# Optimization experiments

Hardware: AMD Instinct MI355X
Metric: run time of the kernel (lower is better)

## Reference

```python
import jax, jax.numpy as jnp
import numpy as np

LN_EPS = 1e-5

def setup_inputs() -> dict:
    key = jax.random.key(0)
    ks = jax.random.split(key, 8)
    B, L, D, H = 4, 2048, 512, 8
    x = jax.random.normal(ks[0], (B, L, D), dtype=jnp.float32)
    token_ids = jax.random.randint(ks[1], (B, L), 0, 50000, dtype=jnp.int64)
    s = 1.0 / np.sqrt(D)
    Wq = jax.random.normal(ks[2], (D, D), dtype=jnp.float32) * s
    Wk = jax.random.normal(ks[3], (D, D), dtype=jnp.float32) * s
    Wv = jax.random.normal(ks[4], (D, D), dtype=jnp.float32) * s
    Wo = jax.random.normal(ks[5], (D, D), dtype=jnp.float32) * s
    gamma = jnp.ones((D,), dtype=jnp.float32)
    beta = jnp.zeros((D,), dtype=jnp.float32)
    return {"x": x, "token_ids": token_ids, "Wq": Wq, "Wk": Wk,
            "Wv": Wv, "Wo": Wo, "gamma": gamma, "beta": beta}

def reference(x, token_ids, Wq, Wk, Wv, Wo, gamma, beta):
    B, L, D = x.shape
    H = 8
    Dh = D // H
    residual = x
    # Pre-LN
    mu = jnp.mean(x, axis=-1, keepdims=True)
    var = jnp.mean(jnp.square(x - mu), axis=-1, keepdims=True)
    xn = (x - mu) * jax.lax.rsqrt(var + LN_EPS) * gamma + beta
    # projections (torch Linear: y = x @ W.T), split heads -> [B,H,L,Dh]
    def proj(W):
        return jnp.einsum('bld,ed->ble', xn, W).reshape(B, L, H, Dh).transpose(0, 2, 1, 3)
    Q, K, V = proj(Wq), proj(Wk), proj(Wv)
    scale = jnp.sqrt(jnp.float32(Dh))
    scores = jnp.einsum('bhqd,bhkd->bhqk', Q, K) / scale  # [B,H,L,L]
    neg_inf = jnp.float32(-jnp.inf)
    causal = jnp.triu(jnp.ones((L, L), dtype=bool), k=1)           # [L,L]
    pad = (token_ids == 0)[:, None, None, :]                       # [B,1,1,L]
    scores = jnp.where(causal[None, None], neg_inf, scores)
    scores = jnp.where(pad, neg_inf, scores)
    all_masked = jnp.all(jnp.isinf(scores), axis=-1, keepdims=True)
    scores = jnp.where(all_masked, 0.0, scores)
    attn = jax.nn.softmax(scores, axis=-1)  # dropout is identity in eval
    out = jnp.einsum('bhqk,bhkd->bhqd', attn, V)
    out = out.transpose(0, 2, 1, 3).reshape(B, L, D)
    out = jnp.einsum('bld,ed->ble', out, Wo)
    return residual + out
```

## Files before the change

### kernel.cpp

```cpp
#include <hip/hip_runtime.h>
#include <math.h>

typedef unsigned short u16;
typedef unsigned int u32;
typedef unsigned long long u64;
typedef float f32x4 __attribute__((ext_vector_type(4)));
typedef __bf16 bf16x8 __attribute__((ext_vector_type(8)));
typedef __bf16 bf16x4 __attribute__((ext_vector_type(4)));

constexpr int Bc = 4, Lc = 2048, Dc = 512, Hc = 8, DHc = 64;
constexpr int NTOK = Bc * Lc;
constexpr float LN_EPS = 1e-5f;
constexpr int KS = 72;
constexpr int PS = 72;
constexpr float QSCALE = 0.125f * 1.44269504088896340736f;

__device__ inline u16 bf_bits(float f) {
  return __builtin_bit_cast(u16, (__bf16)f);
}

__global__ __launch_bounds__(256) void cvt4_kernel(const float* __restrict__ s0,
                                                   const float* __restrict__ s1,
                                                   const float* __restrict__ s2,
                                                   const float* __restrict__ s3,
                                                   u16* __restrict__ d0,
                                                   u16* __restrict__ d1,
                                                   u16* __restrict__ d2,
                                                   u16* __restrict__ d3) {
  int mat = blockIdx.x >> 8;
  int i = ((blockIdx.x & 255) * 256 + threadIdx.x) * 4;
  const float* s = (mat == 0) ? s0 : (mat == 1) ? s1 : (mat == 2) ? s2 : s3;
  u16* d = (mat == 0) ? d0 : (mat == 1) ? d1 : (mat == 2) ? d2 : d3;
  float4 v = *(const float4*)&s[i];
  bf16x4 o;
  o[0] = (__bf16)v.x; o[1] = (__bf16)v.y; o[2] = (__bf16)v.z; o[3] = (__bf16)v.w;
  *(bf16x4*)&d[i] = o;
}

__global__ __launch_bounds__(256) void pmask_kernel(const int* __restrict__ tok,
                                                    u64* __restrict__ pm) {
  int wid = (blockIdx.x * 256 + threadIdx.x) >> 6;
  int lane = threadIdx.x & 63;
  u64 m = __ballot(tok[(size_t)wid * 64 + lane] == 0);
  if (lane == 0) pm[wid] = m;
}

__global__ __launch_bounds__(256) void ln_kernel(const float* __restrict__ x,
                                                 const float* __restrict__ gamma,
                                                 const float* __restrict__ beta,
                                                 u16* __restrict__ xn) {
  int wave = threadIdx.x >> 6;
  int lane = threadIdx.x & 63;
  int row  = blockIdx.x * 4 + wave;
  const float* xr = x + (size_t)row * Dc;
  float4 v0 = ((const float4*)xr)[lane * 2];
  float4 v1 = ((const float4*)xr)[lane * 2 + 1];
  float sum = v0.x + v0.y + v0.z + v0.w + v1.x + v1.y + v1.z + v1.w;
  float sq  = v0.x*v0.x + v0.y*v0.y + v0.z*v0.z + v0.w*v0.w
            + v1.x*v1.x + v1.y*v1.y + v1.z*v1.z + v1.w*v1.w;
  #pragma unroll
  for (int off = 32; off > 0; off >>= 1) {
    sum += __shfl_xor(sum, off);
    sq  += __shfl_xor(sq, off);
  }
  float mu = sum * (1.0f / Dc);
  float rs = rsqrtf(sq * (1.0f / Dc) - mu * mu + LN_EPS);
  float4 g0 = ((const float4*)gamma)[lane * 2];
  float4 g1 = ((const float4*)gamma)[lane * 2 + 1];
  float4 b0 = ((const float4*)beta)[lane * 2];
  float4 b1 = ((const float4*)beta)[lane * 2 + 1];
  bf16x8 o;
  o[0] = (__bf16)((v0.x - mu) * rs * g0.x + b0.x);
  o[1] = (__bf16)((v0.y - mu) * rs * g0.y + b0.y);
  o[2] = (__bf16)((v0.z - mu) * rs * g0.z + b0.z);
  o[3] = (__bf16)((v0.w - mu) * rs * g0.w + b0.w);
  o[4] = (__bf16)((v1.x - mu) * rs * g1.x + b1.x);
  o[5] = (__bf16)((v1.y - mu) * rs * g1.y + b1.y);
  o[6] = (__bf16)((v1.z - mu) * rs * g1.z + b1.z);
  o[7] = (__bf16)((v1.w - mu) * rs * g1.w + b1.w);
  *(bf16x8*)&xn[(size_t)row * Dc + lane * 8] = o;
}

template <int MODE>
__global__ __launch_bounds__(256) void gemm_bf16(const u16* __restrict__ A,
                                                 const u16* __restrict__ W,
                                                 const float* __restrict__ res,
                                                 float* __restrict__ out_f,
                                                 u16* __restrict__ o_q,
                                                 u16* __restrict__ o_k,
                                                 u16* __restrict__ o_v,
                                                 float* __restrict__ vm) {
  __shared__ u16 As[128 * KS];
  __shared__ u16 Bs[128 * KS];
  int tid = threadIdx.x;
  int lane = tid & 63;
  int w = tid >> 6;
  int wr = w >> 1, wc = w & 1;
  int cc = lane & 15, rb = lane >> 4;
  int n0 = blockIdx.x * 128;
  int e0 = blockIdx.y * 128;
  f32x4 acc[4][4] = {};
  for (int k0 = 0; k0 < Dc; k0 += 64) {
    #pragma unroll
    for (int u = 0; u < 4; u++) {
      int idx = u * 256 + tid;
      int row = idx >> 3;
      int col = (idx & 7) << 3;
      *(uint4*)&As[row * KS + col] = *(const uint4*)&A[(size_t)(n0 + row) * Dc + k0 + col];
      *(uint4*)&Bs[row * KS + col] = *(const uint4*)&W[(size_t)(e0 + row) * Dc + k0 + col];
    }
    __syncthreads();
    #pragma unroll
    for (int kk = 0; kk < 64; kk += 32) {
      bf16x8 aF[4], bF[4];
      #pragma unroll
      for (int m = 0; m < 4; m++)
        aF[m] = *(bf16x8*)&As[(wr * 64 + m * 16 + cc) * KS + kk + rb * 8];
      #pragma unroll
      for (int n = 0; n < 4; n++)
        bF[n] = *(bf16x8*)&Bs[(wc * 64 + n * 16 + cc) * KS + kk + rb * 8];
      #pragma unroll
      for (int m = 0; m < 4; m++)
        #pragma unroll
        for (int n = 0; n < 4; n++)
          acc[m][n] = __builtin_amdgcn_mfma_f32_16x16x32_bf16(aF[m], bF[n], acc[m][n], 0, 0, 0);
    }
    __syncthreads();
  }
  if (MODE == 3) {
    int bb = n0 >> 11;
    #pragma unroll
    for (int n = 0; n < 4; n++) {
      int c = e0 + wc * 64 + n * 16 + cc;
      int mat = c >> 9;
      int cm = c & 511;
      int h = cm >> 6, dh = cm & 63;
      if (mat == 2) {
        float cp = 0.f;
        #pragma unroll
        for (int m = 0; m < 4; m++) {
          int l0 = (n0 + wr * 64 + m * 16 + rb * 4) & (Lc - 1);
          bf16x4 o4;
          o4[0] = (__bf16)acc[m][n][0]; o4[1] = (__bf16)acc[m][n][1];
          o4[2] = (__bf16)acc[m][n][2]; o4[3] = (__bf16)acc[m][n][3];
          *(bf16x4*)&o_v[((size_t)(bb * Hc + h) * DHc + dh) * Lc + l0] = o4;
          cp += (acc[m][n][0] + acc[m][n][1]) + (acc[m][n][2] + acc[m][n][3]);
        }
        cp += __shfl_xor(cp, 16);
        cp += __shfl_xor(cp, 32);
        if (lane < 16) atomicAdd(&vm[(bb * Hc + h) * DHc + dh], cp);
      } else {
        u16* dst = (mat == 0) ? o_q : o_k;
        float sc = (mat == 0) ? QSCALE : 1.0f;
        #pragma unroll
        for (int m = 0; m < 4; m++) {
          #pragma unroll
          for (int j = 0; j < 4; j++) {
            int r = n0 + wr * 64 + m * 16 + rb * 4 + j;
            int ll = r & (Lc - 1);
            dst[(((size_t)(bb * Hc + h)) * Lc + ll) * DHc + dh] = bf_bits(acc[m][n][j] * sc);
          }
        }
      }
    }
  } else {
    #pragma unroll
    for (int m = 0; m < 4; m++) {
      #pragma unroll
      for (int n = 0; n < 4; n++) {
        #pragma unroll
        for (int j = 0; j < 4; j++) {
          int r = n0 + wr * 64 + m * 16 + rb * 4 + j;
          int c = e0 + wc * 64 + n * 16 + cc;
          size_t o = (size_t)r * Dc + c;
          out_f[o] = acc[m][n][j] + res[o];
        }
      }
    }
  }
}

__global__ __launch_bounds__(64) void attn3(const u16* __restrict__ Q,
                                            const u16* __restrict__ K,
                                            const u16* __restrict__ VT,
                                            const float* __restrict__ vm,
                                            const u64* __restrict__ pmask,
                                            u16* __restrict__ out) {
  __shared__ u16 Ps[32 * PS];
  int lane = threadIdx.x;
  int cc = lane & 15, rb = lane >> 4;
  int bh = blockIdx.x;
  int qt = (int)gridDim.y - 1 - (int)blockIdx.y;
  int q0 = qt * 32;
  int b = bh >> 3, h = bh & 7;
  const u16* Qb = Q + (size_t)bh * Lc * DHc;
  const u16* Kb = K + (size_t)bh * Lc * DHc;
  const u16* Vb = VT + (size_t)bh * DHc * Lc;
  const u64* pmb = pmask + (b << 5);

  bf16x8 qF[2][2];
  #pragma unroll
  for (int qb = 0; qb < 2; qb++)
    #pragma unroll
    for (int kc = 0; kc < 2; kc++)
      qF[qb][kc] = *(const bf16x8*)&Qb[(size_t)(q0 + qb * 16 + cc) * DHc + kc * 32 + rb * 8];

  float mrow[2] = {-INFINITY, -INFINITY};
  float lrow[2] = {0.f, 0.f};
  f32x4 acc[2][4] = {};
  int nfull = q0 >> 6;

  bf16x8 kf[4][2];
  #pragma unroll
  for (int c = 0; c < 4; c++) {
    const u16* kp = &Kb[(size_t)(c * 16 + cc) * DHc + rb * 8];
    kf[c][0] = *(const bf16x8*)kp;
    kf[c][1] = *(const bf16x8*)(kp + 32);
  }

  for (int kt = 0; kt <= nfull; kt++) {
    int k0 = kt * 64;
    bool last = (kt == nfull);
    u64 pm = pmb[kt];
    bf16x8 vf[2][4];
    #pragma unroll
    for (int kc = 0; kc < 2; kc++)
      #pragma unroll
      for (int d0 = 0; d0 < 4; d0++)
        vf[kc][d0] = *(const bf16x8*)&Vb[(size_t)(d0 * 16 + cc) * Lc + k0 + kc * 32 + rb * 8];

    f32x4 sq[2][4] = {};
    __builtin_amdgcn_s_setprio(1);
    #pragma unroll
    for (int c = 0; c < 4; c++) {
      #pragma unroll
      for (int qb = 0; qb < 2; qb++) {
        sq[qb][c] = __builtin_amdgcn_mfma_f32_16x16x32_bf16(kf[c][0], qF[qb][0], sq[qb][c], 0, 0, 0);
        sq[qb][c] = __builtin_amdgcn_mfma_f32_16x16x32_bf16(kf[c][1], qF[qb][1], sq[qb][c], 0, 0, 0);
      }
    }
    __builtin_amdgcn_s_setprio(0);
    if (!last) {
      #pragma unroll
      for (int c = 0; c < 4; c++) {
        const u16* kp = &Kb[(size_t)(k0 + 64 + c * 16 + cc) * DHc + rb * 8];
        kf[c][0] = *(const bf16x8*)kp;
        kf[c][1] = *(const bf16x8*)(kp + 32);
      }
    }
    #pragma unroll
    for (int c = 0; c < 4; c++) {
      u32 smr = (((u32)(pm >> (c * 16)) & 0xffffu) >> (rb * 4));
      #pragma unroll
      for (int qb = 0; qb < 2; qb++)
        #pragma unroll
        for (int j = 0; j < 4; j++)
          if ((smr >> j) & 1) sq[qb][c][j] = -INFINITY;
    }
    if (last) {
      #pragma unroll
      for (int qb = 0; qb < 2; qb++) {
        int qrel = q0 + qb * 16 + cc - k0;
        #pragma unroll
        for (int c = 0; c < 4; c++)
          #pragma unroll
          for (int j = 0; j < 4; j++)
            if (c * 16 + rb * 4 + j > qrel) sq[qb][c][j] = -INFINITY;
      }
    }
    #pragma unroll
    for (int qb = 0; qb < 2; qb++) {
      float m0 = fmaxf(fmaxf(sq[qb][0][0], sq[qb][0][1]), fmaxf(sq[qb][0][2], sq[qb][0][3]));
      float m1 = fmaxf(fmaxf(sq[qb][1][0], sq[qb][1][1]), fmaxf(sq[qb][1][2], sq[qb][1][3]));
      float m2 = fmaxf(fmaxf(sq[qb][2][0], sq[qb][2][1]), fmaxf(sq[qb][2][2], sq[qb][2][3]));
      float m3 = fmaxf(fmaxf(sq[qb][3][0], sq[qb][3][1]), fmaxf(sq[qb][3][2], sq[qb][3][3]));
      float mx = fmaxf(fmaxf(m0, m1), fmaxf(m2, m3));
      mx = fmaxf(mx, __shfl_xor(mx, 16));
      mx = fmaxf(mx, __shfl_xor(mx, 32));
      if (!__all(mx <= mrow[qb] + 8.f)) {
        float nm = fmaxf(mrow[qb], mx);
        float nm2 = fmaxf(nm, -1e30f);
        float alpha = exp2f(mrow[qb] - nm2);
        lrow[qb] *= alpha;
        #pragma unroll
        for (int d0 = 0; d0 < 4; d0++)
          #pragma unroll
          for (int j = 0; j < 4; j++)
            acc[qb][d0][j] *= alpha;
        mrow[qb] = nm;
      }
      float nm2 = fmaxf(mrow[qb], -1e30f);
      float rs = 0.f;
      #pragma unroll
      for (int c = 0; c < 4; c++) {
        f32x4 p;
        #pragma unroll
        for (int j = 0; j < 4; j++) p[j] = exp2f(sq[qb][c][j] - nm2);
        rs += (p[0] + p[1]) + (p[2] + p[3]);
        bf16x4 p4;
        p4[0] = (__bf16)p[0]; p4[1] = (__bf16)p[1];
        p4[2] = (__bf16)p[2]; p4[3] = (__bf16)p[3];
        *(bf16x4*)&Ps[(qb * 16 + cc) * PS + c * 16 + rb * 4] = p4;
      }
      rs += __shfl_xor(rs, 16);
      rs += __shfl_xor(rs, 32);
      lrow[qb] += rs;
    }
    asm volatile("s_waitcnt lgkmcnt(0)" ::: "memory");
    __builtin_amdgcn_sched_barrier(0);
    __builtin_amdgcn_s_setprio(1);
    #pragma unroll
    for (int kc = 0; kc < 2; kc++) {
      bf16x8 pF0 = *(bf16x8*)&Ps[(size_t)cc * PS + kc * 32 + rb * 8];
      bf16x8 pF1 = *(bf16x8*)&Ps[(size_t)(16 + cc) * PS + kc * 32 + rb * 8];
      #pragma unroll
      for (int d0 = 0; d0 < 4; d0++) {
        acc[0][d0] = __builtin_amdgcn_mfma_f32_16x16x32_bf16(vf[kc][d0], pF0, acc[0][d0], 0, 0, 0);
        acc[1][d0] = __builtin_amdgcn_mfma_f32_16x16x32_bf16(vf[kc][d0], pF1, acc[1][d0], 0, 0, 0);
      }
    }
    __builtin_amdgcn_s_setprio(0);
  }
  #pragma unroll
  for (int qb = 0; qb < 2; qb++) {
    int q = q0 + qb * 16 + cc;
    bool ok = lrow[qb] > 0.f;
    float inv = ok ? 1.0f / lrow[qb] : 0.f;
    #pragma unroll
    for (int d0 = 0; d0 < 4; d0++) {
      bf16x4 o4;
      #pragma unroll
      for (int j = 0; j < 4; j++) {
        float v = ok ? acc[qb][d0][j] * inv
                     : vm[bh * DHc + d0 * 16 + rb * 4 + j] * (1.0f / Lc);
        o4[j] = (__bf16)v;
      }
      *(bf16x4*)&out[((size_t)(b * Lc + q)) * Dc + h * DHc + d0 * 16 + rb * 4] = o4;
    }
  }
}

extern "C" void kernel_launch(void* const* d_in, const int* in_sizes, int n_in,
                              void* d_out, int out_size, void* d_ws, size_t ws_size,
                              hipStream_t stream) {
  const float* x     = (const float*)d_in[0];
  const int*   tok   = (const int*)d_in[1];
  const float* Wq    = (const float*)d_in[2];
  const float* Wk    = (const float*)d_in[3];
  const float* Wv    = (const float*)d_in[4];
  const float* Wo    = (const float*)d_in[5];
  const float* gamma = (const float*)d_in[6];
  const float* beta  = (const float*)d_in[7];
  float* out = (float*)d_out;

  const size_t SEG = (size_t)NTOK * Dc;
  const size_t WSEG = (size_t)Dc * Dc;
  u16* xn   = (u16*)d_ws;
  u16* Qd   = xn + SEG;
  u16* Kd   = Qd + SEG;
  u16* VT   = Kd + SEG;
  u16* ao   = VT + SEG;
  u16* Wqkv = ao + SEG;
  u16* Wob  = Wqkv + 3 * WSEG;
  float* vm = (float*)(Wob + WSEG);
  u64* pmarr = (u64*)(vm + (size_t)Bc * Hc * DHc);

  (void)hipMemsetAsync(vm, 0, (size_t)Bc * Hc * DHc * sizeof(float), stream);

  cvt4_kernel<<<1024, 256, 0, stream>>>(Wq, Wk, Wv, Wo,
                                        Wqkv, Wqkv + WSEG, Wqkv + 2 * WSEG, Wob);
  ln_kernel<<<NTOK / 4, 256, 0, stream>>>(x, gamma, beta, xn);
  pmask_kernel<<<32, 256, 0, stream>>>(tok, pmarr);

  dim3 gq(NTOK / 128, (3 * Dc) / 128);
  gemm_bf16<3><<<gq, 256, 0, stream>>>(xn, Wqkv, nullptr, nullptr, Qd, Kd, VT, vm);

  dim3 ga(Bc * Hc, Lc / 32);
  attn3<<<ga, 64, 0, stream>>>(Qd, Kd, VT, vm, pmarr, ao);

  dim3 gg(NTOK / 128, Dc / 128);
  gemm_bf16<0><<<gg, 256, 0, stream>>>(ao, Wob, x, out, nullptr, nullptr, nullptr, nullptr);
}
```

Baseline: 123.5 us.

## Share K/V tiles across four waves via double-buffered async LDS staging

The attention kernel goes from one wave per 32-query tile to four waves per 128-query block. The waves share K and V tiles staged into XOR-swizzled LDS with async global_load_lds double buffering, instead of each wave reading K/V from global memory itself. The V projection output is rewritten into a 64x64-blocked transposed layout so each tile is one contiguous 8KB chunk, and the weight-convert and pad-mask kernels are merged into one launch. This cuts redundant global K/V traffic and one launch. In exchange it adds per-tile block barriers, and waves with fewer causal tiles sit idle while their neighbours finish.

```diff
diff --git a/kernel.cpp b/kernel.cpp
--- a/kernel.cpp
+++ b/kernel.cpp
@@ -19,30 +19,32 @@
   return __builtin_bit_cast(u16, (__bf16)f);
 }
 
-__global__ __launch_bounds__(256) void cvt4_kernel(const float* __restrict__ s0,
+__global__ __launch_bounds__(256) void prep_kernel(const float* __restrict__ s0,
                                                    const float* __restrict__ s1,
                                                    const float* __restrict__ s2,
                                                    const float* __restrict__ s3,
                                                    u16* __restrict__ d0,
                                                    u16* __restrict__ d1,
                                                    u16* __restrict__ d2,
-                                                   u16* __restrict__ d3) {
-  int mat = blockIdx.x >> 8;
-  int i = ((blockIdx.x & 255) * 256 + threadIdx.x) * 4;
-  const float* s = (mat == 0) ? s0 : (mat == 1) ? s1 : (mat == 2) ? s2 : s3;
-  u16* d = (mat == 0) ? d0 : (mat == 1) ? d1 : (mat == 2) ? d2 : d3;
-  float4 v = *(const float4*)&s[i];
-  bf16x4 o;
-  o[0] = (__bf16)v.x; o[1] = (__bf16)v.y; o[2] = (__bf16)v.z; o[3] = (__bf16)v.w;
-  *(bf16x4*)&d[i] = o;
-}
-
-__global__ __launch_bounds__(256) void pmask_kernel(const int* __restrict__ tok,
-                                                    u64* __restrict__ pm) {
-  int wid = (blockIdx.x * 256 + threadIdx.x) >> 6;
-  int lane = threadIdx.x & 63;
-  u64 m = __ballot(tok[(size_t)wid * 64 + lane] == 0);
-  if (lane == 0) pm[wid] = m;
+                                                   u16* __restrict__ d3,
+                                                   const int* __restrict__ tok,
+                                                   u64* __restrict__ pm) {
+  int bid = blockIdx.x;
+  if (bid < 1024) {
+    int mat = bid >> 8;
+    int i = ((bid & 255) * 256 + threadIdx.x) * 4;
+    const float* s = (mat == 0) ? s0 : (mat == 1) ? s1 : (mat == 2) ? s2 : s3;
+    u16* d = (mat == 0) ? d0 : (mat == 1) ? d1 : (mat == 2) ? d2 : d3;
+    float4 v = *(const float4*)&s[i];
+    bf16x4 o;
+    o[0] = (__bf16)v.x; o[1] = (__bf16)v.y; o[2] = (__bf16)v.z; o[3] = (__bf16)v.w;
+    *(bf16x4*)&d[i] = o;
+  } else {
+    int wid = ((bid - 1024) * 256 + threadIdx.x) >> 6;
+    int lane = threadIdx.x & 63;
+    u64 m = __ballot(tok[(size_t)wid * 64 + lane] == 0);
+    if (lane == 0) pm[wid] = m;
+  }
 }
 
 __global__ __launch_bounds__(256) void ln_kernel(const float* __restrict__ x,
@@ -129,36 +131,41 @@
   }
   if (MODE == 3) {
     int bb = n0 >> 11;
-    #pragma unroll
-    for (int n = 0; n < 4; n++) {
-      int c = e0 + wc * 64 + n * 16 + cc;
-      int mat = c >> 9;
-      int cm = c & 511;
-      int h = cm >> 6, dh = cm & 63;
-      if (mat == 2) {
+    int mat = e0 >> 9;
+    int e0c = e0 & 511;
+    if (mat == 2) {
+      #pragma unroll
+      for (int n = 0; n < 4; n++) {
+        int c = e0c + wc * 64 + n * 16 + cc;
+        int h = c >> 6, dh = c & 63;
         float cp = 0.f;
         #pragma unroll
         for (int m = 0; m < 4; m++) {
-          int l0 = (n0 + wr * 64 + m * 16 + rb * 4) & (Lc - 1);
+          int l = (n0 + wr * 64 + m * 16 + rb * 4) & (Lc - 1);
           bf16x4 o4;
           o4[0] = (__bf16)acc[m][n][0]; o4[1] = (__bf16)acc[m][n][1];
           o4[2] = (__bf16)acc[m][n][2]; o4[3] = (__bf16)acc[m][n][3];
-          *(bf16x4*)&o_v[((size_t)(bb * Hc + h) * DHc + dh) * Lc + l0] = o4;
+          size_t addr = ((((size_t)(bb * Hc + h)) * (Lc / 64) + (l >> 6)) * DHc + dh) * 64 + (l & 63);
+          *(bf16x4*)&o_v[addr] = o4;
           cp += (acc[m][n][0] + acc[m][n][1]) + (acc[m][n][2] + acc[m][n][3]);
         }
         cp += __shfl_xor(cp, 16);
         cp += __shfl_xor(cp, 32);
         if (lane < 16) atomicAdd(&vm[(bb * Hc + h) * DHc + dh], cp);
-      } else {
-        u16* dst = (mat == 0) ? o_q : o_k;
-        float sc = (mat == 0) ? QSCALE : 1.0f;
-        #pragma unroll
-        for (int m = 0; m < 4; m++) {
+      }
+    } else {
+      float sc = (mat == 0) ? QSCALE : 1.0f;
+      u16* dst = (mat == 0) ? o_q : o_k;
+      #pragma unroll
+      for (int m = 0; m < 4; m++) {
+        #pragma unroll
+        for (int n = 0; n < 4; n++) {
           #pragma unroll
           for (int j = 0; j < 4; j++) {
             int r = n0 + wr * 64 + m * 16 + rb * 4 + j;
+            int c = e0c + wc * 64 + n * 16 + cc;
             int ll = r & (Lc - 1);
-            dst[(((size_t)(bb * Hc + h)) * Lc + ll) * DHc + dh] = bf_bits(acc[m][n][j] * sc);
+            dst[(((size_t)(bb * Hc + (c >> 6))) * Lc + ll) * DHc + (c & 63)] = bf_bits(acc[m][n][j] * sc);
           }
         }
       }
@@ -180,23 +187,29 @@
   }
 }
 
-__global__ __launch_bounds__(64) void attn3(const u16* __restrict__ Q,
-                                            const u16* __restrict__ K,
-                                            const u16* __restrict__ VT,
-                                            const float* __restrict__ vm,
-                                            const u64* __restrict__ pmask,
-                                            u16* __restrict__ out) {
-  __shared__ u16 Ps[32 * PS];
-  int lane = threadIdx.x;
+__global__ __launch_bounds__(256) void attn5(const u16* __restrict__ Q,
+                                             const u16* __restrict__ K,
+                                             const u16* __restrict__ VT,
+                                             const float* __restrict__ vm,
+                                             const u64* __restrict__ pmask,
+                                             u16* __restrict__ out) {
+  __shared__ u16 Ksh[2][4096];
+  __shared__ u16 Vsh[2][4096];
+  __shared__ u16 Ps[4][32 * PS];
+  int tid = threadIdx.x;
+  int w = tid >> 6;
+  int lane = tid & 63;
   int cc = lane & 15, rb = lane >> 4;
   int bh = blockIdx.x;
-  int qt = (int)gridDim.y - 1 - (int)blockIdx.y;
-  int q0 = qt * 32;
+  int qblk = (int)gridDim.y - 1 - (int)blockIdx.y;
+  int q0 = qblk * 128 + w * 32;
   int b = bh >> 3, h = bh & 7;
   const u16* Qb = Q + (size_t)bh * Lc * DHc;
   const u16* Kb = K + (size_t)bh * Lc * DHc;
-  const u16* Vb = VT + (size_t)bh * DHc * Lc;
+  const u16* Vb = VT + (size_t)bh * Lc * DHc;
   const u64* pmb = pmask + (b << 5);
+  int own_last = q0 >> 6;
+  int NT = 2 * qblk + 2;
 
   bf16x8 qF[2][2];
   #pragma unroll
@@ -208,119 +221,137 @@
   float mrow[2] = {-INFINITY, -INFINITY};
   float lrow[2] = {0.f, 0.f};
   f32x4 acc[2][4] = {};
-  int nfull = q0 >> 6;
-
-  bf16x8 kf[4][2];
-  #pragma unroll
-  for (int c = 0; c < 4; c++) {
-    const u16* kp = &Kb[(size_t)(c * 16 + cc) * DHc + rb * 8];
-    kf[c][0] = *(const bf16x8*)kp;
-    kf[c][1] = *(const bf16x8*)(kp + 32);
-  }
-
-  for (int kt = 0; kt <= nfull; kt++) {
-    int k0 = kt * 64;
-    bool last = (kt == nfull);
-    u64 pm = pmb[kt];
-    bf16x8 vf[2][4];
-    #pragma unroll
-    for (int kc = 0; kc < 2; kc++)
-      #pragma unroll
-      for (int d0 = 0; d0 < 4; d0++)
-        vf[kc][d0] = *(const bf16x8*)&Vb[(size_t)(d0 * 16 + cc) * Lc + k0 + kc * 32 + rb * 8];
-
-    f32x4 sq[2][4] = {};
-    __builtin_amdgcn_s_setprio(1);
-    #pragma unroll
-    for (int c = 0; c < 4; c++) {
+
+  auto stage = [&](int kt, int buf) {
+    const char* gK = (const char*)(Kb + (size_t)kt * 64 * DHc);
+    const char* gV = (const char*)(Vb + (size_t)kt * 4096);
+    #pragma unroll
+    for (int i = 0; i < 2; i++) {
+      int s = (i * 4 + w) * 64 + lane;
+      int row = s >> 3;
+      int src = row * 128 + (((s & 7) ^ (row & 7)) << 4);
+      u16* lK = &Ksh[buf][(i * 4 + w) * 512];
+      u16* lV = &Vsh[buf][(i * 4 + w) * 512];
+      __builtin_amdgcn_global_load_lds(
+          (const __attribute__((address_space(1))) void*)(gK + src),
+          (__attribute__((address_space(3))) void*)lK, 16, 0, 0);
+      __builtin_amdgcn_global_load_lds(
+          (const __attribute__((address_space(1))) void*)(gV + src),
+          (__attribute__((address_space(3))) void*)lV, 16, 0, 0);
+    }
+  };
+
+  stage(0, 0);
+  for (int kt = 0; kt < NT; kt++) {
+    int cur = kt & 1;
+    bool more = (kt + 1 < NT);
+    if (more) stage(kt + 1, cur ^ 1);
+    if (more) asm volatile("s_waitcnt vmcnt(4)" ::: "memory");
+    else      asm volatile("s_waitcnt vmcnt(0)" ::: "memory");
+    __builtin_amdgcn_sched_barrier(0);
+    __builtin_amdgcn_s_barrier();
+    __builtin_amdgcn_sched_barrier(0);
+
+    if (kt <= own_last) {
+      const u16* Kl = Ksh[cur];
+      const u16* Vl = Vsh[cur];
+      bool last = (kt == own_last);
+      u64 pm = pmb[kt];
+      int sw = cc & 7;
+      f32x4 sq[2][4] = {};
+      #pragma unroll
+      for (int c = 0; c < 4; c++) {
+        int krow = c * 16 + cc;
+        bf16x8 kf0 = *(const bf16x8*)&Kl[krow * 64 + ((rb ^ sw) << 3)];
+        bf16x8 kf1 = *(const bf16x8*)&Kl[krow * 64 + (((rb + 4) ^ sw) << 3)];
+        __builtin_amdgcn_s_setprio(1);
+        #pragma unroll
+        for (int qb = 0; qb < 2; qb++) {
+          sq[qb][c] = __builtin_amdgcn_mfma_f32_16x16x32_bf16(kf0, qF[qb][0], sq[qb][c], 0, 0, 0);
+          sq[qb][c] = __builtin_amdgcn_mfma_f32_16x16x32_bf16(kf1, qF[qb][1], sq[qb][c], 0, 0, 0);
+        }
+        __builtin_amdgcn_s_setprio(0);
+      }
+      if (pm) {
+        #pragma unroll
+        for (int c = 0; c < 4; c++) {
+          u32 smr = (((u32)(pm >> (c * 16)) & 0xffffu) >> (rb * 4));
+          #pragma unroll
+          for (int qb = 0; qb < 2; qb++)
+            #pragma unroll
+            for (int j = 0; j < 4; j++)
+              if ((smr >> j) & 1) sq[qb][c][j] = -INFINITY;
+        }
+      }
+      if (last) {
+        #pragma unroll
+        for (int qb = 0; qb < 2; qb++) {
+          int qrel = q0 + qb * 16 + cc - kt * 64;
+          #pragma unroll
+          for (int c = 0; c < 4; c++)
+            #pragma unroll
+            for (int j = 0; j < 4; j++)
+              if (c * 16 + rb * 4 + j > qrel) sq[qb][c][j] = -INFINITY;
+        }
+      }
       #pragma unroll
       for (int qb = 0; qb < 2; qb++) {
-        sq[qb][c] = __builtin_amdgcn_mfma_f32_16x16x32_bf16(kf[c][0], qF[qb][0], sq[qb][c], 0, 0, 0);
-        sq[qb][c] = __builtin_amdgcn_mfma_f32_16x16x32_bf16(kf[c][1], qF[qb][1], sq[qb][c], 0, 0, 0);
-      }
-    }
-    __builtin_amdgcn_s_setprio(0);
-    if (!last) {
-      #pragma unroll
-      for (int c = 0; c < 4; c++) {
-        const u16* kp = &Kb[(size_t)(k0 + 64 + c * 16 + cc) * DHc + rb * 8];
-        kf[c][0] = *(const bf16x8*)kp;
-        kf[c][1] = *(const bf16x8*)(kp + 32);
-      }
-    }
-    #pragma unroll
-    for (int c = 0; c < 4; c++) {
-      u32 smr = (((u32)(pm >> (c * 16)) & 0xffffu) >> (rb * 4));
-      #pragma unroll
-      for (int qb = 0; qb < 2; qb++)
-        #pragma unroll
-        for (int j = 0; j < 4; j++)
-          if ((smr >> j) & 1) sq[qb][c][j] = -INFINITY;
-    }
-    if (last) {
-      #pragma unroll
-      for (int qb = 0; qb < 2; qb++) {
-        int qrel = q0 + qb * 16 + cc - k0;
-        #pragma unroll
-        for (int c = 0; c < 4; c++)
+        float m0 = fmaxf(fmaxf(sq[qb][0][0], sq[qb][0][1]), fmaxf(sq[qb][0][2], sq[qb][0][3]));
+        float m1 = fmaxf(fmaxf(sq[qb][1][0], sq[qb][1][1]), fmaxf(sq[qb][1][2], sq[qb][1][3]));
+        float m2 = fmaxf(fmaxf(sq[qb][2][0], sq[qb][2][1]), fmaxf(sq[qb][2][2], sq[qb][2][3]));
+        float m3 = fmaxf(fmaxf(sq[qb][3][0], sq[qb][3][1]), fmaxf(sq[qb][3][2], sq[qb][3][3]));
+        float mx = fmaxf(fmaxf(m0, m1), fmaxf(m2, m3));
+        mx = fmaxf(mx, __shfl_xor(mx, 16));
+        mx = fmaxf(mx, __shfl_xor(mx, 32));
+        if (!__all(mx <= mrow[qb] + 8.f)) {
+          float nm = fmaxf(mrow[qb], mx);
+          float nm2 = fmaxf(nm, -1e30f);
+          float alpha = exp2f(mrow[qb] - nm2);
+          lrow[qb] *= alpha;
           #pragma unroll
-          for (int j = 0; j < 4; j++)
-            if (c * 16 + rb * 4 + j > qrel) sq[qb][c][j] = -INFINITY;
-      }
-    }
-    #pragma unroll
-    for (int qb = 0; qb < 2; qb++) {
-      float m0 = fmaxf(fmaxf(sq[qb][0][0], sq[qb][0][1]), fmaxf(sq[qb][0][2], sq[qb][0][3]));
-      float m1 = fmaxf(fmaxf(sq[qb][1][0], sq[qb][1][1]), fmaxf(sq[qb][1][2], sq[qb][1][3]));
-      float m2 = fmaxf(fmaxf(sq[qb][2][0], sq[qb][2][1]), fmaxf(sq[qb][2][2], sq[qb][2][3]));
-      float m3 = fmaxf(fmaxf(sq[qb][3][0], sq[qb][3][1]), fmaxf(sq[qb][3][2], sq[qb][3][3]));
-      float mx = fmaxf(fmaxf(m0, m1), fmaxf(m2, m3));
-      mx = fmaxf(mx, __shfl_xor(mx, 16));
-      mx = fmaxf(mx, __shfl_xor(mx, 32));
-      if (!__all(mx <= mrow[qb] + 8.f)) {
-        float nm = fmaxf(mrow[qb], mx);
-        float nm2 = fmaxf(nm, -1e30f);
-        float alpha = exp2f(mrow[qb] - nm2);
-        lrow[qb] *= alpha;
-        #pragma unroll
-        for (int d0 = 0; d0 < 4; d0++)
+          for (int d0 = 0; d0 < 4; d0++)
+            #pragma unroll
+            for (int j = 0; j < 4; j++)
+              acc[qb][d0][j] *= alpha;
+          mrow[qb] = nm;
+        }
+        float nm2 = fmaxf(mrow[qb], -1e30f);
+        float rs = 0.f;
+        #pragma unroll
+        for (int c = 0; c < 4; c++) {
+          f32x4 p;
           #pragma unroll
-          for (int j = 0; j < 4; j++)
-            acc[qb][d0][j] *= alpha;
-        mrow[qb] = nm;
-      }
-      float nm2 = fmaxf(mrow[qb], -1e30f);
-      float rs = 0.f;
-      #pragma unroll
-      for (int c = 0; c < 4; c++) {
-        f32x4 p;
-        #pragma unroll
-        for (int j = 0; j < 4; j++) p[j] = exp2f(sq[qb][c][j] - nm2);
-        rs += (p[0] + p[1]) + (p[2] + p[3]);
-        bf16x4 p4;
-        p4[0] = (__bf16)p[0]; p4[1] = (__bf16)p[1];
-        p4[2] = (__bf16)p[2]; p4[3] = (__bf16)p[3];
-        *(bf16x4*)&Ps[(qb * 16 + cc) * PS + c * 16 + rb * 4] = p4;
-      }
-      rs += __shfl_xor(rs, 16);
-      rs += __shfl_xor(rs, 32);
-      lrow[qb] += rs;
-    }
-    asm volatile("s_waitcnt lgkmcnt(0)" ::: "memory");
-    __builtin_amdgcn_sched_barrier(0);
-    __builtin_amdgcn_s_setprio(1);
-    #pragma unroll
-    for (int kc = 0; kc < 2; kc++) {
-      bf16x8 pF0 = *(bf16x8*)&Ps[(size_t)cc * PS + kc * 32 + rb * 8];
-      bf16x8 pF1 = *(bf16x8*)&Ps[(size_t)(16 + cc) * PS + kc * 32 + rb * 8];
-      #pragma unroll
-      for (int d0 = 0; d0 < 4; d0++) {
-        acc[0][d0] = __builtin_amdgcn_mfma_f32_16x16x32_bf16(vf[kc][d0], pF0, acc[0][d0], 0, 0, 0);
-        acc[1][d0] = __builtin_amdgcn_mfma_f32_16x16x32_bf16(vf[kc][d0], pF1, acc[1][d0], 0, 0, 0);
-      }
-    }
-    __builtin_amdgcn_s_setprio(0);
-  }
+          for (int j = 0; j < 4; j++) p[j] = exp2f(sq[qb][c][j] - nm2);
+          rs += (p[0] + p[1]) + (p[2] + p[3]);
+          bf16x4 p4;
+          p4[0] = (__bf16)p[0]; p4[1] = (__bf16)p[1];
+          p4[2] = (__bf16)p[2]; p4[3] = (__bf16)p[3];
+          *(bf16x4*)&Ps[w][(qb * 16 + cc) * PS + c * 16 + rb * 4] = p4;
+        }
+        rs += __shfl_xor(rs, 16);
+        rs += __shfl_xor(rs, 32);
+        lrow[qb] += rs;
+      }
+      asm volatile("s_waitcnt lgkmcnt(0)" ::: "memory");
+      __builtin_amdgcn_sched_barrier(0);
+      __builtin_amdgcn_s_setprio(1);
+      #pragma unroll
+      for (int kc = 0; kc < 2; kc++) {
+        bf16x8 pF0 = *(bf16x8*)&Ps[w][(size_t)cc * PS + kc * 32 + rb * 8];
+        bf16x8 pF1 = *(bf16x8*)&Ps[w][(size_t)(16 + cc) * PS + kc * 32 + rb * 8];
+        #pragma unroll
+        for (int d0 = 0; d0 < 4; d0++) {
+          int vrow = d0 * 16 + cc;
+          bf16x8 vfv = *(const bf16x8*)&Vl[vrow * 64 + (((kc * 4 + rb) ^ sw) << 3)];
+          acc[0][d0] = __builtin_amdgcn_mfma_f32_16x16x32_bf16(vfv, pF0, acc[0][d0], 0, 0, 0);
+          acc[1][d0] = __builtin_amdgcn_mfma_f32_16x16x32_bf16(vfv, pF1, acc[1][d0], 0, 0, 0);
+        }
+      }
+      __builtin_amdgcn_s_setprio(0);
+    }
+    __syncthreads();
+  }
+
   #pragma unroll
   for (int qb = 0; qb < 2; qb++) {
     int q = q0 + qb * 16 + cc;
@@ -367,16 +398,16 @@
 
   (void)hipMemsetAsync(vm, 0, (size_t)Bc * Hc * DHc * sizeof(float), stream);
 
-  cvt4_kernel<<<1024, 256, 0, stream>>>(Wq, Wk, Wv, Wo,
-                                        Wqkv, Wqkv + WSEG, Wqkv + 2 * WSEG, Wob);
+  prep_kernel<<<1056, 256, 0, stream>>>(Wq, Wk, Wv, Wo,
+                                        Wqkv, Wqkv + WSEG, Wqkv + 2 * WSEG, Wob,
+                                        tok, pmarr);
   ln_kernel<<<NTOK / 4, 256, 0, stream>>>(x, gamma, beta, xn);
-  pmask_kernel<<<32, 256, 0, stream>>>(tok, pmarr);
 
   dim3 gq(NTOK / 128, (3 * Dc) / 128);
   gemm_bf16<3><<<gq, 256, 0, stream>>>(xn, Wqkv, nullptr, nullptr, Qd, Kd, VT, vm);
 
-  dim3 ga(Bc * Hc, Lc / 32);
-  attn3<<<ga, 64, 0, stream>>>(Qd, Kd, VT, vm, pmarr, ao);
+  dim3 ga(Bc * Hc, Lc / 128);
+  attn5<<<ga, 256, 0, stream>>>(Qd, Kd, VT, vm, pmarr, ao);
 
   dim3 gg(NTOK / 128, Dc / 128);
   gemm_bf16<0><<<gg, 256, 0, stream>>>(ao, Wob, x, out, nullptr, nullptr, nullptr, nullptr);
```

Result: slower. 127.4 us (+3.1%).

## Split long causal attention rows into KV chunks with a separate merge kernel

Applied to the files above, without the earlier changes.

Attention for later query tiles is split across up to four KV chunks of 8 tiles each. Partial bf16 outputs plus running max and sum are written to a workspace, and a new merge kernel combines them. This balances work across blocks, since causal rows otherwise get longer with query index. V is stored in a tiled [tile][dh][64] layout so each tile reads contiguously. The weight-conversion and pad-mask kernels are merged into one launch, and pad masking is skipped when a tile has no pad tokens. The cost is an extra launch plus partial-result traffic, and bf16 partials add some rounding error.

```diff
diff --git a/kernel.cpp b/kernel.cpp
--- a/kernel.cpp
+++ b/kernel.cpp
@@ -14,35 +14,38 @@
 constexpr int KS = 72;
 constexpr int PS = 72;
 constexpr float QSCALE = 0.125f * 1.44269504088896340736f;
+constexpr int PSLOT = 2176;
 
 __device__ inline u16 bf_bits(float f) {
   return __builtin_bit_cast(u16, (__bf16)f);
 }
 
-__global__ __launch_bounds__(256) void cvt4_kernel(const float* __restrict__ s0,
+__global__ __launch_bounds__(256) void prep_kernel(const float* __restrict__ s0,
                                                    const float* __restrict__ s1,
                                                    const float* __restrict__ s2,
                                                    const float* __restrict__ s3,
                                                    u16* __restrict__ d0,
                                                    u16* __restrict__ d1,
                                                    u16* __restrict__ d2,
-                                                   u16* __restrict__ d3) {
-  int mat = blockIdx.x >> 8;
-  int i = ((blockIdx.x & 255) * 256 + threadIdx.x) * 4;
-  const float* s = (mat == 0) ? s0 : (mat == 1) ? s1 : (mat == 2) ? s2 : s3;
-  u16* d = (mat == 0) ? d0 : (mat == 1) ? d1 : (mat == 2) ? d2 : d3;
-  float4 v = *(const float4*)&s[i];
-  bf16x4 o;
-  o[0] = (__bf16)v.x; o[1] = (__bf16)v.y; o[2] = (__bf16)v.z; o[3] = (__bf16)v.w;
-  *(bf16x4*)&d[i] = o;
-}
-
-__global__ __launch_bounds__(256) void pmask_kernel(const int* __restrict__ tok,
-                                                    u64* __restrict__ pm) {
-  int wid = (blockIdx.x * 256 + threadIdx.x) >> 6;
-  int lane = threadIdx.x & 63;
-  u64 m = __ballot(tok[(size_t)wid * 64 + lane] == 0);
-  if (lane == 0) pm[wid] = m;
+                                                   u16* __restrict__ d3,
+                                                   const int* __restrict__ tok,
+                                                   u64* __restrict__ pm) {
+  int bid = blockIdx.x;
+  if (bid < 1024) {
+    int mat = bid >> 8;
+    int i = ((bid & 255) * 256 + threadIdx.x) * 4;
+    const float* s = (mat == 0) ? s0 : (mat == 1) ? s1 : (mat == 2) ? s2 : s3;
+    u16* d = (mat == 0) ? d0 : (mat == 1) ? d1 : (mat == 2) ? d2 : d3;
+    float4 v = *(const float4*)&s[i];
+    bf16x4 o;
+    o[0] = (__bf16)v.x; o[1] = (__bf16)v.y; o[2] = (__bf16)v.z; o[3] = (__bf16)v.w;
+    *(bf16x4*)&d[i] = o;
+  } else {
+    int wid = ((bid - 1024) * 256 + threadIdx.x) >> 6;
+    int lane = threadIdx.x & 63;
+    u64 m = __ballot(tok[(size_t)wid * 64 + lane] == 0);
+    if (lane == 0) pm[wid] = m;
+  }
 }
 
 __global__ __launch_bounds__(256) void ln_kernel(const float* __restrict__ x,
@@ -129,36 +132,41 @@
   }
   if (MODE == 3) {
     int bb = n0 >> 11;
-    #pragma unroll
-    for (int n = 0; n < 4; n++) {
-      int c = e0 + wc * 64 + n * 16 + cc;
-      int mat = c >> 9;
-      int cm = c & 511;
-      int h = cm >> 6, dh = cm & 63;
-      if (mat == 2) {
+    int mat = e0 >> 9;
+    int e0c = e0 & 511;
+    if (mat == 2) {
+      #pragma unroll
+      for (int n = 0; n < 4; n++) {
+        int c = e0c + wc * 64 + n * 16 + cc;
+        int h = c >> 6, dh = c & 63;
         float cp = 0.f;
         #pragma unroll
         for (int m = 0; m < 4; m++) {
-          int l0 = (n0 + wr * 64 + m * 16 + rb * 4) & (Lc - 1);
+          int l = (n0 + wr * 64 + m * 16 + rb * 4) & (Lc - 1);
           bf16x4 o4;
           o4[0] = (__bf16)acc[m][n][0]; o4[1] = (__bf16)acc[m][n][1];
           o4[2] = (__bf16)acc[m][n][2]; o4[3] = (__bf16)acc[m][n][3];
-          *(bf16x4*)&o_v[((size_t)(bb * Hc + h) * DHc + dh) * Lc + l0] = o4;
+          size_t addr = ((((size_t)(bb * Hc + h)) * (Lc / 64) + (l >> 6)) * DHc + dh) * 64 + (l & 63);
+          *(bf16x4*)&o_v[addr] = o4;
           cp += (acc[m][n][0] + acc[m][n][1]) + (acc[m][n][2] + acc[m][n][3]);
         }
         cp += __shfl_xor(cp, 16);
         cp += __shfl_xor(cp, 32);
         if (lane < 16) atomicAdd(&vm[(bb * Hc + h) * DHc + dh], cp);
-      } else {
-        u16* dst = (mat == 0) ? o_q : o_k;
-        float sc = (mat == 0) ? QSCALE : 1.0f;
-        #pragma unroll
-        for (int m = 0; m < 4; m++) {
+      }
+    } else {
+      float sc = (mat == 0) ? QSCALE : 1.0f;
+      u16* dst = (mat == 0) ? o_q : o_k;
+      #pragma unroll
+      for (int m = 0; m < 4; m++) {
+        #pragma unroll
+        for (int n = 0; n < 4; n++) {
           #pragma unroll
           for (int j = 0; j < 4; j++) {
             int r = n0 + wr * 64 + m * 16 + rb * 4 + j;
+            int c = e0c + wc * 64 + n * 16 + cc;
             int ll = r & (Lc - 1);
-            dst[(((size_t)(bb * Hc + h)) * Lc + ll) * DHc + dh] = bf_bits(acc[m][n][j] * sc);
+            dst[(((size_t)(bb * Hc + (c >> 6))) * Lc + ll) * DHc + (c & 63)] = bf_bits(acc[m][n][j] * sc);
           }
         }
       }
@@ -180,22 +188,32 @@
   }
 }
 
-__global__ __launch_bounds__(64) void attn3(const u16* __restrict__ Q,
+__global__ __launch_bounds__(64) void attn6(const u16* __restrict__ Q,
                                             const u16* __restrict__ K,
                                             const u16* __restrict__ VT,
                                             const float* __restrict__ vm,
                                             const u64* __restrict__ pmask,
-                                            u16* __restrict__ out) {
+                                            u16* __restrict__ out,
+                                            u16* __restrict__ part) {
   __shared__ u16 Ps[32 * PS];
   int lane = threadIdx.x;
   int cc = lane & 15, rb = lane >> 4;
   int bh = blockIdx.x;
-  int qt = (int)gridDim.y - 1 - (int)blockIdx.y;
+  int y = blockIdx.y;
+  int qt, ch;
+  if (y < 16)      { qt = y;                 ch = 0; }
+  else if (y < 48) { qt = 16 + ((y - 16) >> 1); ch = (y - 16) & 1; }
+  else if (y < 96) { qt = 32 + (y - 48) / 3;    ch = (y - 48) % 3; }
+  else             { qt = 48 + ((y - 96) >> 2); ch = (y - 96) & 3; }
   int q0 = qt * 32;
+  int own_last = qt >> 1;
+  int t = own_last + 1;
+  int k_lo = ch * 8;
+  int k_hi = (k_lo + 8 < t) ? k_lo + 8 : t;
   int b = bh >> 3, h = bh & 7;
   const u16* Qb = Q + (size_t)bh * Lc * DHc;
   const u16* Kb = K + (size_t)bh * Lc * DHc;
-  const u16* Vb = VT + (size_t)bh * DHc * Lc;
+  const u16* Vb = VT + (size_t)bh * Lc * DHc;
   const u64* pmb = pmask + (b << 5);
 
   bf16x8 qF[2][2];
@@ -208,26 +226,28 @@
   float mrow[2] = {-INFINITY, -INFINITY};
   float lrow[2] = {0.f, 0.f};
   f32x4 acc[2][4] = {};
-  int nfull = q0 >> 6;
 
   bf16x8 kf[4][2];
-  #pragma unroll
-  for (int c = 0; c < 4; c++) {
-    const u16* kp = &Kb[(size_t)(c * 16 + cc) * DHc + rb * 8];
-    kf[c][0] = *(const bf16x8*)kp;
-    kf[c][1] = *(const bf16x8*)(kp + 32);
-  }
-
-  for (int kt = 0; kt <= nfull; kt++) {
+  {
+    const u16* kp = Kb + (size_t)(k_lo * 64) * DHc;
+    #pragma unroll
+    for (int c = 0; c < 4; c++) {
+      kf[c][0] = *(const bf16x8*)&kp[(c * 16 + cc) * DHc + rb * 8];
+      kf[c][1] = *(const bf16x8*)&kp[(c * 16 + cc) * DHc + 32 + rb * 8];
+    }
+  }
+
+  for (int kt = k_lo; kt < k_hi; kt++) {
     int k0 = kt * 64;
-    bool last = (kt == nfull);
+    bool last = (kt == own_last);
     u64 pm = pmb[kt];
+    const u16* vp = Vb + (size_t)kt * (DHc * 64);
     bf16x8 vf[2][4];
     #pragma unroll
     for (int kc = 0; kc < 2; kc++)
       #pragma unroll
       for (int d0 = 0; d0 < 4; d0++)
-        vf[kc][d0] = *(const bf16x8*)&Vb[(size_t)(d0 * 16 + cc) * Lc + k0 + kc * 32 + rb * 8];
+        vf[kc][d0] = *(const bf16x8*)&vp[(d0 * 16 + cc) * 64 + kc * 32 + rb * 8];
 
     f32x4 sq[2][4] = {};
     __builtin_amdgcn_s_setprio(1);
@@ -240,22 +260,24 @@
       }
     }
     __builtin_amdgcn_s_setprio(0);
-    if (!last) {
+    if (kt + 1 < k_hi) {
+      const u16* kp = Kb + (size_t)(k0 + 64) * DHc;
       #pragma unroll
       for (int c = 0; c < 4; c++) {
-        const u16* kp = &Kb[(size_t)(k0 + 64 + c * 16 + cc) * DHc + rb * 8];
-        kf[c][0] = *(const bf16x8*)kp;
-        kf[c][1] = *(const bf16x8*)(kp + 32);
-      }
-    }
-    #pragma unroll
-    for (int c = 0; c < 4; c++) {
-      u32 smr = (((u32)(pm >> (c * 16)) & 0xffffu) >> (rb * 4));
-      #pragma unroll
-      for (int qb = 0; qb < 2; qb++)
-        #pragma unroll
-        for (int j = 0; j < 4; j++)
-          if ((smr >> j) & 1) sq[qb][c][j] = -INFINITY;
+        kf[c][0] = *(const bf16x8*)&kp[(c * 16 + cc) * DHc + rb * 8];
+        kf[c][1] = *(const bf16x8*)&kp[(c * 16 + cc) * DHc + 32 + rb * 8];
+      }
+    }
+    if (pm) {
+      #pragma unroll
+      for (int c = 0; c < 4; c++) {
+        u32 smr = (((u32)(pm >> (c * 16)) & 0xffffu) >> (rb * 4));
+        #pragma unroll
+        for (int qb = 0; qb < 2; qb++)
+          #pragma unroll
+          for (int j = 0; j < 4; j++)
+            if ((smr >> j) & 1) sq[qb][c][j] = -INFINITY;
+      }
     }
     if (last) {
       #pragma unroll
@@ -321,22 +343,94 @@
     }
     __builtin_amdgcn_s_setprio(0);
   }
+
+  if (y < 16) {
+    #pragma unroll
+    for (int qb = 0; qb < 2; qb++) {
+      int q = q0 + qb * 16 + cc;
+      bool ok = lrow[qb] > 0.f;
+      float inv = ok ? 1.0f / lrow[qb] : 0.f;
+      #pragma unroll
+      for (int d0 = 0; d0 < 4; d0++) {
+        bf16x4 o4;
+        #pragma unroll
+        for (int j = 0; j < 4; j++) {
+          float v = ok ? acc[qb][d0][j] * inv
+                       : vm[bh * DHc + d0 * 16 + rb * 4 + j] * (1.0f / Lc);
+          o4[j] = (__bf16)v;
+        }
+        *(bf16x4*)&out[((size_t)(b * Lc + q)) * Dc + h * DHc + d0 * 16 + rb * 4] = o4;
+      }
+    }
+  } else {
+    int sb = bh * 144 + 2 * qt - 32
+           + ((qt >= 32) ? qt - 32 : 0) + ((qt >= 48) ? qt - 48 : 0) + ch;
+    u16* pp = part + (size_t)sb * PSLOT;
+    #pragma unroll
+    for (int qb = 0; qb < 2; qb++) {
+      #pragma unroll
+      for (int d0 = 0; d0 < 4; d0++) {
+        bf16x4 o4;
+        #pragma unroll
+        for (int j = 0; j < 4; j++) o4[j] = (__bf16)acc[qb][d0][j];
+        *(bf16x4*)&pp[(qb * 16 + cc) * 64 + d0 * 16 + rb * 4] = o4;
+      }
+      if (rb == 0) {
+        float* pml = (float*)(pp + 2048);
+        pml[qb * 16 + cc] = mrow[qb];
+        pml[32 + qb * 16 + cc] = lrow[qb];
+      }
+    }
+  }
+}
+
+__global__ __launch_bounds__(64) void attn_merge(const u16* __restrict__ part,
+                                                 const float* __restrict__ vm,
+                                                 u16* __restrict__ out) {
+  int lane = threadIdx.x;
+  int q = lane & 31, half = lane >> 5;
+  int bh = blockIdx.x;
+  int qt = 16 + (int)blockIdx.y;
+  int b = bh >> 3, h = bh & 7;
+  int nch = 2 + (qt >= 32) + (qt >= 48);
+  int sb = bh * 144 + 2 * qt - 32
+         + ((qt >= 32) ? qt - 32 : 0) + ((qt >= 48) ? qt - 48 : 0);
+  const u16* p0 = part + (size_t)sb * PSLOT;
+  float M = -INFINITY;
+  for (int i = 0; i < nch; i++) {
+    const float* pml = (const float*)(p0 + i * PSLOT + 2048);
+    M = fmaxf(M, pml[q]);
+  }
+  float nm2 = fmaxf(M, -1e30f);
+  float o[32];
   #pragma unroll
-  for (int qb = 0; qb < 2; qb++) {
-    int q = q0 + qb * 16 + cc;
-    bool ok = lrow[qb] > 0.f;
-    float inv = ok ? 1.0f / lrow[qb] : 0.f;
-    #pragma unroll
-    for (int d0 = 0; d0 < 4; d0++) {
-      bf16x4 o4;
-      #pragma unroll
-      for (int j = 0; j < 4; j++) {
-        float v = ok ? acc[qb][d0][j] * inv
-                     : vm[bh * DHc + d0 * 16 + rb * 4 + j] * (1.0f / Lc);
-        o4[j] = (__bf16)v;
-      }
-      *(bf16x4*)&out[((size_t)(b * Lc + q)) * Dc + h * DHc + d0 * 16 + rb * 4] = o4;
-    }
+  for (int u = 0; u < 32; u++) o[u] = 0.f;
+  float L = 0.f;
+  for (int i = 0; i < nch; i++) {
+    const float* pml = (const float*)(p0 + i * PSLOT + 2048);
+    float a = exp2f(pml[q] - nm2);
+    L += a * pml[32 + q];
+    const u16* pa = p0 + i * PSLOT + q * 64 + half * 32;
+    #pragma unroll
+    for (int u = 0; u < 8; u++) {
+      bf16x4 v = *(const bf16x4*)&pa[u * 4];
+      #pragma unroll
+      for (int j = 0; j < 4; j++) o[u * 4 + j] += a * (float)v[j];
+    }
+  }
+  bool ok = L > 0.f;
+  float inv = ok ? 1.0f / L : 0.f;
+  u16* dst = out + ((size_t)(b * Lc + qt * 32 + q)) * Dc + h * DHc + half * 32;
+  #pragma unroll
+  for (int u = 0; u < 8; u++) {
+    bf16x4 o4;
+    #pragma unroll
+    for (int j = 0; j < 4; j++) {
+      float v = ok ? o[u * 4 + j] * inv
+                   : vm[bh * DHc + half * 32 + u * 4 + j] * (1.0f / Lc);
+      o4[j] = (__bf16)v;
+    }
+    *(bf16x4*)&dst[u * 4] = o4;
   }
 }
 
@@ -364,19 +458,22 @@
   u16* Wob  = Wqkv + 3 * WSEG;
   float* vm = (float*)(Wob + WSEG);
   u64* pmarr = (u64*)(vm + (size_t)Bc * Hc * DHc);
+  u16* part = (u16*)(pmarr + 128);
 
   (void)hipMemsetAsync(vm, 0, (size_t)Bc * Hc * DHc * sizeof(float), stream);
 
-  cvt4_kernel<<<1024, 256, 0, stream>>>(Wq, Wk, Wv, Wo,
-                                        Wqkv, Wqkv + WSEG, Wqkv + 2 * WSEG, Wob);
+  prep_kernel<<<1056, 256, 0, stream>>>(Wq, Wk, Wv, Wo,
+                                        Wqkv, Wqkv + WSEG, Wqkv + 2 * WSEG, Wob,
+                                        tok, pmarr);
   ln_kernel<<<NTOK / 4, 256, 0, stream>>>(x, gamma, beta, xn);
-  pmask_kernel<<<32, 256, 0, stream>>>(tok, pmarr);
 
   dim3 gq(NTOK / 128, (3 * Dc) / 128);
   gemm_bf16<3><<<gq, 256, 0, stream>>>(xn, Wqkv, nullptr, nullptr, Qd, Kd, VT, vm);
 
-  dim3 ga(Bc * Hc, Lc / 32);
-  attn3<<<ga, 64, 0, stream>>>(Qd, Kd, VT, vm, pmarr, ao);
+  dim3 ga(Bc * Hc, 160);
+  attn6<<<ga, 64, 0, stream>>>(Qd, Kd, VT, vm, pmarr, ao, part);
+  dim3 gm(Bc * Hc, 48);
+  attn_merge<<<gm, 64, 0, stream>>>(part, vm, ao);
 
   dim3 gg(NTOK / 128, Dc / 128);
   gemm_bf16<0><<<gg, 256, 0, stream>>>(ao, Wob, x, out, nullptr, nullptr, nullptr, nullptr);
```

Result: slower. 137.7 us (+11.5%).
